# Kernel tuning notes

Hardware: AMD Instinct MI355X
Metric: run time of the kernel (lower is better)

Reference implementation:

```python
import jax, jax.numpy as jnp
import numpy as np

N = 100000   # nodes
E = 1600000  # edges
F = 256      # feature_dim
H = 64       # hidden_dim == out_channels
HEADS = 1


def setup_inputs() -> dict:
    key = jax.random.key(0)
    ks = jax.random.split(key, 12)
    x = jax.random.normal(ks[0], (N, F), dtype=jnp.float32)
    edge_index = jax.random.randint(ks[1], (2, E), 0, N, dtype=jnp.int32)
    s = 0.05
    params = {
        'W_proj': jax.random.normal(ks[2], (F, H), dtype=jnp.float32) * s,
        'b_proj': jnp.zeros((H,), dtype=jnp.float32),
        'Wq1': jax.random.normal(ks[3], (H, HEADS * H), dtype=jnp.float32) * s,
        'Wk1': jax.random.normal(ks[4], (H, HEADS * H), dtype=jnp.float32) * s,
        'Wv1': jax.random.normal(ks[5], (H, HEADS * H), dtype=jnp.float32) * s,
        'Wq2': jax.random.normal(ks[6], (H, HEADS * H), dtype=jnp.float32) * s,
        'Wk2': jax.random.normal(ks[7], (H, HEADS * H), dtype=jnp.float32) * s,
        'Wv2': jax.random.normal(ks[8], (H, HEADS * H), dtype=jnp.float32) * s,
        'W_sig': jax.random.normal(ks[9], (H, 1), dtype=jnp.float32) * s,
        'b_sig': jnp.zeros((1,), dtype=jnp.float32),
    }
    return {'x': x, 'edge_index': edge_index, **params}


def _gat_layer(x, src, dst, Wq, Wk, Wv):
    # x: [N, H]; src/dst: [E] (edge_index[0]=source j, edge_index[1]=dest i)
    n = x.shape[0]
    q = (x @ Wq).reshape(n, HEADS, H)
    k = (x @ Wk).reshape(n, HEADS, H)
    v = (x @ Wv).reshape(n, HEADS, H)
    # edge-wise scores: (q_i * k_j).sum(-1) / sqrt(out_channels)
    scores = jnp.einsum('ehc,ehc->eh', q[dst], k[src]) / np.float32(np.sqrt(H))
    alpha = jax.nn.relu(scores)                                  # [E, HEADS]
    # segment softmax over destination neighborhoods (numerically stable)
    m = jax.ops.segment_max(alpha, dst, num_segments=n)          # [N, HEADS]
    m = jnp.where(jnp.isfinite(m), m, jnp.float32(0.0))
    e = jnp.exp(alpha - m[dst])
    denom = jax.ops.segment_sum(e, dst, num_segments=n)
    a = e / (denom[dst] + jnp.float32(1e-16))                    # [E, HEADS]
    # scatter-weighted sum of values to destinations
    out = jax.ops.segment_sum(v[src] * a[:, :, None], dst, num_segments=n)
    return out.mean(axis=1), a                                   # [N, H], [E, HEADS]


def reference(x, edge_index, W_proj, b_proj, Wq1, Wk1, Wv1, Wq2, Wk2, Wv2, W_sig, b_sig):
    src, dst = edge_index[0], edge_index[1]
    h = jax.nn.gelu(x @ W_proj + b_proj, approximate=False)
    h, attn1 = _gat_layer(h, src, dst, Wq1, Wk1, Wv1)
    h = jax.nn.gelu(h, approximate=False)
    h, attn2 = _gat_layer(h, src, dst, Wq2, Wk2, Wv2)
    signals = h @ W_sig + b_sig                                  # [N, 1]
    return signals, attn1, attn2
```

## Files before the change

### kernel.cpp

```cpp
#include <hip/hip_runtime.h>
#include <hip/hip_fp16.h>
#include <math.h>

#define FF 256
#define HH 64

typedef __attribute__((ext_vector_type(8))) short short8;
typedef __attribute__((ext_vector_type(4))) float f32x4;

__device__ __forceinline__ float gelu_f(float x) {
    float ax = fabsf(x) * 0.70710678118654752f;
    float t = __builtin_amdgcn_rcpf(fmaf(0.3275911f, ax, 1.0f));
    float poly = t * fmaf(t, fmaf(t, fmaf(t, fmaf(t, 1.061405429f, -1.453152027f),
                  1.421413741f), -0.284496736f), 0.254829592f);
    float er = 1.0f - poly * __expf(-ax * ax);
    er = (x < 0.f) ? -er : er;
    return 0.5f * x * (1.0f + er);
}

__device__ __forceinline__ unsigned short bf16rne(float f) {
    unsigned u = __float_as_uint(f);
    unsigned r = u + 0x7FFFu + ((u >> 16) & 1u);
    return (unsigned short)(r >> 16);
}

__device__ __forceinline__ void bf16split(float f, short& hi, short& lo) {
    unsigned u = __float_as_uint(f);
    unsigned r = u + 0x7FFFu + ((u >> 16) & 1u);
    hi = (short)(r >> 16);
    float fh = __uint_as_float(r & 0xFFFF0000u);
    float fl = f - fh;
    unsigned u2 = __float_as_uint(fl);
    unsigned r2 = u2 + 0x7FFFu + ((u2 >> 16) & 1u);
    lo = (short)(r2 >> 16);
}

__device__ __forceinline__ __half2 shfl_xor_h2(__half2 v, int off) {
    union { __half2 h; int i; } u;
    u.h = v;
    u.i = __shfl_xor(u.i, off, 64);
    return u.h;
}

__global__ __launch_bounds__(256) void k_wprep(
        const float* __restrict__ Wp,
        const float* __restrict__ Wq1, const float* __restrict__ Wk1, const float* __restrict__ Wv1,
        const float* __restrict__ Wq2, const float* __restrict__ Wk2, const float* __restrict__ Wv2,
        short* __restrict__ wf) {
    int total = 16384 + 6 * 4096;
    for (int gid = blockIdx.x * 256 + threadIdx.x; gid < total; gid += gridDim.x * 256) {
        const float* W;
        int fid, hibase, lobase;
        if (gid < 16384) {
            W = Wp; fid = gid; hibase = 0; lobase = 16384;
        } else {
            int t = gid - 16384;
            int m = t >> 12;
            fid = t & 4095;
            switch (m) {
                case 0: W = Wq1; break;
                case 1: W = Wk1; break;
                case 2: W = Wv1; break;
                case 3: W = Wq2; break;
                case 4: W = Wk2; break;
                default: W = Wv2; break;
            }
            hibase = 32768 + m * 8192;
            lobase = hibase + 4096;
        }
        int j    = fid & 7;
        int lane = (fid >> 3) & 63;
        int ct   = (fid >> 9) & 3;
        int s    = fid >> 11;
        int k    = s * 32 + (lane >> 4) * 8 + j;
        int col  = ct * 16 + (lane & 15);
        short hi, lo;
        bf16split(W[k * HH + col], hi, lo);
        wf[hibase + fid] = hi;
        wf[lobase + fid] = lo;
    }
}

__device__ __forceinline__ void do_degree(int bid, const int* __restrict__ dst,
        int* __restrict__ deg, int* __restrict__ rank, int E) {
    int e0 = (bid * 256 + threadIdx.x) * 4;
    if (e0 + 3 < E) {
        int4 d4 = *reinterpret_cast<const int4*>(dst + e0);
        int4 r4;
        r4.x = atomicAdd(&deg[d4.x], 1);
        r4.y = atomicAdd(&deg[d4.y], 1);
        r4.z = atomicAdd(&deg[d4.z], 1);
        r4.w = atomicAdd(&deg[d4.w], 1);
        *reinterpret_cast<int4*>(rank + e0) = r4;
    } else {
        for (int e = e0; e < E; ++e) rank[e] = atomicAdd(&deg[dst[e]], 1);
    }
}

__device__ __forceinline__ void do_fill(int bid, const int* __restrict__ src,
        const int* __restrict__ dst, const int* __restrict__ rowptr,
        const int* __restrict__ rank,
        int* __restrict__ esrc, int* __restrict__ inv, int E) {
    int e0 = (bid * 256 + threadIdx.x) * 4;
    if (e0 + 3 < E) {
        int4 d4 = *reinterpret_cast<const int4*>(dst + e0);
        int4 s4 = *reinterpret_cast<const int4*>(src + e0);
        int4 r4 = *reinterpret_cast<const int4*>(rank + e0);
        int p0 = rowptr[d4.x] + r4.x;
        int p1 = rowptr[d4.y] + r4.y;
        int p2 = rowptr[d4.z] + r4.z;
        int p3 = rowptr[d4.w] + r4.w;
        esrc[p0] = s4.x;
        esrc[p1] = s4.y;
        esrc[p2] = s4.z;
        esrc[p3] = s4.w;
        *reinterpret_cast<int4*>(inv + e0) = (int4){p0, p1, p2, p3};
    } else {
        for (int e = e0; e < E; ++e) {
            int pos = rowptr[dst[e]] + rank[e];
            esrc[pos] = src[e];
            inv[e] = pos;
        }
    }
}

__device__ __forceinline__ void do_attn(int bid, const float* __restrict__ ecsr,
        const int* __restrict__ inv, float* __restrict__ attn, int E) {
    int e0 = (bid * 256 + threadIdx.x) * 4;
    if (e0 + 3 < E) {
        int4 i4 = *reinterpret_cast<const int4*>(inv + e0);
        float4 a;
        a.x = ecsr[i4.x]; a.y = ecsr[i4.y]; a.z = ecsr[i4.z]; a.w = ecsr[i4.w];
        *reinterpret_cast<float4*>(attn + e0) = a;
    } else {
        for (int e = e0; e < E; ++e) attn[e] = ecsr[inv[e]];
    }
}

__device__ __forceinline__ void do_proj(int bid, const float* __restrict__ x,
        const short* __restrict__ wf, const float* __restrict__ b,
        float* __restrict__ h, int n) {
    if (bid * 64 >= n) return;
    int lane = threadIdx.x & 63;
    int w    = threadIdx.x >> 6;
    int m    = lane & 15, g = lane >> 4;
    int rowc = min(bid * 64 + w * 16 + m, n - 1);
    const float* xrow = x + (size_t)rowc * FF + g * 8;
    const short* wlo = wf + 16384;
    f32x4 acc[4];
    #pragma unroll
    for (int ct = 0; ct < 4; ++ct) acc[ct] = (f32x4){0.f, 0.f, 0.f, 0.f};
    #pragma unroll
    for (int s = 0; s < 8; ++s) {
        float4 a0 = *reinterpret_cast<const float4*>(xrow + s * 32);
        float4 a1 = *reinterpret_cast<const float4*>(xrow + s * 32 + 4);
        float av[8] = {a0.x, a0.y, a0.z, a0.w, a1.x, a1.y, a1.z, a1.w};
        short8 ah, al;
        #pragma unroll
        for (int j = 0; j < 8; ++j) { short hi, lo; bf16split(av[j], hi, lo); ah[j] = hi; al[j] = lo; }
        #pragma unroll
        for (int ct = 0; ct < 4; ++ct) {
            int fo = ((s * 4 + ct) * 64 + lane) * 8;
            short8 bh = *reinterpret_cast<const short8*>(wf + fo);
            short8 bl = *reinterpret_cast<const short8*>(wlo + fo);
            acc[ct] = __builtin_amdgcn_mfma_f32_16x16x32_bf16(ah, bh, acc[ct], 0, 0, 0);
            acc[ct] = __builtin_amdgcn_mfma_f32_16x16x32_bf16(al, bh, acc[ct], 0, 0, 0);
            acc[ct] = __builtin_amdgcn_mfma_f32_16x16x32_bf16(ah, bl, acc[ct], 0, 0, 0);
        }
    }
    int orow0 = bid * 64 + w * 16 + g * 4;
    #pragma unroll
    for (int ct = 0; ct < 4; ++ct) {
        int col = ct * 16 + m;
        float bias = b[col];
        #pragma unroll
        for (int r = 0; r < 4; ++r) {
            int row = orow0 + r;
            if (row < n) h[(size_t)row * HH + col] = acc[ct][r] + bias;
        }
    }
}

__device__ __forceinline__ void do_qkv(int bid, const float* __restrict__ hsrc,
        const short* __restrict__ wfq, const short* __restrict__ wfk, const short* __restrict__ wfv,
        __half* __restrict__ qh, __half* __restrict__ kv, int n) {
    if (bid * 64 >= n) return;
    int lane = threadIdx.x & 63;
    int w    = threadIdx.x >> 6;
    int m    = lane & 15, g = lane >> 4;
    int rowc = min(bid * 64 + w * 16 + m, n - 1);
    const float* hrow = hsrc + (size_t)rowc * HH + g * 8;
    f32x4 aq[4], ak[4], av_[4];
    #pragma unroll
    for (int ct = 0; ct < 4; ++ct) {
        aq[ct] = (f32x4){0.f, 0.f, 0.f, 0.f};
        ak[ct] = (f32x4){0.f, 0.f, 0.f, 0.f};
        av_[ct] = (f32x4){0.f, 0.f, 0.f, 0.f};
    }
    #pragma unroll
    for (int s = 0; s < 2; ++s) {
        float4 a0 = *reinterpret_cast<const float4*>(hrow + s * 32);
        float4 a1 = *reinterpret_cast<const float4*>(hrow + s * 32 + 4);
        float avv[8] = {a0.x, a0.y, a0.z, a0.w, a1.x, a1.y, a1.z, a1.w};
        short8 ah;
        #pragma unroll
        for (int j = 0; j < 8; ++j) ah[j] = (short)bf16rne(gelu_f(avv[j]));
        #pragma unroll
        for (int ct = 0; ct < 4; ++ct) {
            int fo = ((s * 4 + ct) * 64 + lane) * 8;
            short8 qh8 = *reinterpret_cast<const short8*>(wfq + fo);
            short8 ql8 = *reinterpret_cast<const short8*>(wfq + 4096 + fo);
            short8 kh8 = *reinterpret_cast<const short8*>(wfk + fo);
            short8 kl8 = *reinterpret_cast<const short8*>(wfk + 4096 + fo);
            short8 vh8 = *reinterpret_cast<const short8*>(wfv + fo);
            short8 vl8 = *reinterpret_cast<const short8*>(wfv + 4096 + fo);
            aq[ct] = __builtin_amdgcn_mfma_f32_16x16x32_bf16(ah, qh8, aq[ct], 0, 0, 0);
            aq[ct] = __builtin_amdgcn_mfma_f32_16x16x32_bf16(ah, ql8, aq[ct], 0, 0, 0);
            ak[ct] = __builtin_amdgcn_mfma_f32_16x16x32_bf16(ah, kh8, ak[ct], 0, 0, 0);
            ak[ct] = __builtin_amdgcn_mfma_f32_16x16x32_bf16(ah, kl8, ak[ct], 0, 0, 0);
            av_[ct] = __builtin_amdgcn_mfma_f32_16x16x32_bf16(ah, vh8, av_[ct], 0, 0, 0);
            av_[ct] = __builtin_amdgcn_mfma_f32_16x16x32_bf16(ah, vl8, av_[ct], 0, 0, 0);
        }
    }
    int orow0 = bid * 64 + w * 16 + g * 4;
    #pragma unroll
    for (int ct = 0; ct < 4; ++ct) {
        int col = ct * 16 + m;
        int cb  = (col >> 3) * 16 + (col & 7);
        #pragma unroll
        for (int r = 0; r < 4; ++r) {
            int row = orow0 + r;
            if (row < n) {
                qh[(size_t)row * HH + col]     = __float2half(aq[ct][r]);
                kv[(size_t)row * 128 + cb]     = __float2half(ak[ct][r]);
                kv[(size_t)row * 128 + cb + 8] = __float2half(av_[ct][r]);
            }
        }
    }
}

__global__ __launch_bounds__(256) void k_proj_degree(
        const float* __restrict__ x, const short* __restrict__ wf,
        const float* __restrict__ b, float* __restrict__ h, int n,
        const int* __restrict__ dst, int* __restrict__ deg, int* __restrict__ rank, int E) {
    int bid = blockIdx.x >> 1;
    if ((blockIdx.x & 1) == 0) do_proj(bid, x, wf, b, h, n);
    else                       do_degree(bid, dst, deg, rank, E);
}

__global__ __launch_bounds__(256) void k_qkv_fill(
        const float* __restrict__ hsrc,
        const short* __restrict__ wfq, const short* __restrict__ wfk, const short* __restrict__ wfv,
        __half* __restrict__ qh, __half* __restrict__ kv, int n,
        const int* __restrict__ src, const int* __restrict__ dst,
        const int* __restrict__ rowptr, const int* __restrict__ rank,
        int* __restrict__ esrc, int* __restrict__ inv, int E) {
    int bid = blockIdx.x >> 1;
    if ((blockIdx.x & 1) == 0) do_qkv(bid, hsrc, wfq, wfk, wfv, qh, kv, n);
    else                       do_fill(bid, src, dst, rowptr, rank, esrc, inv, E);
}

__global__ __launch_bounds__(256) void k_qkv_attn(
        const float* __restrict__ hsrc,
        const short* __restrict__ wfq, const short* __restrict__ wfk, const short* __restrict__ wfv,
        __half* __restrict__ qh, __half* __restrict__ kv, int n,
        const float* __restrict__ ecsr, const int* __restrict__ inv,
        float* __restrict__ attn, int E) {
    int bid = blockIdx.x >> 1;
    if ((blockIdx.x & 1) == 0) do_qkv(bid, hsrc, wfq, wfk, wfv, qh, kv, n);
    else                       do_attn(bid, ecsr, inv, attn, E);
}

__global__ __launch_bounds__(256) void k_attn(const float* __restrict__ ecsr,
        const int* __restrict__ inv, float* __restrict__ attn, int E) {
    do_attn(blockIdx.x, ecsr, inv, attn, E);
}

__global__ __launch_bounds__(256) void k_scan1(const int* __restrict__ deg,
        int* __restrict__ out, int* __restrict__ bsums, int n) {
    __shared__ int lds[256];
    int t = threadIdx.x;
    int base = blockIdx.x * 1024 + t * 4;
    int v0 = (base     < n) ? deg[base]     : 0;
    int v1 = (base + 1 < n) ? deg[base + 1] : 0;
    int v2 = (base + 2 < n) ? deg[base + 2] : 0;
    int v3 = (base + 3 < n) ? deg[base + 3] : 0;
    int s = v0 + v1 + v2 + v3;
    int val = s;
    lds[t] = val;
    __syncthreads();
    #pragma unroll
    for (int off = 1; off < 256; off <<= 1) {
        int tmp = (t >= off) ? lds[t - off] : 0;
        __syncthreads();
        val += tmp;
        lds[t] = val;
        __syncthreads();
    }
    if (t == 255) bsums[blockIdx.x] = val;
    int excl = val - s;
    if (base     < n) out[base]     = excl;
    if (base + 1 < n) out[base + 1] = excl + v0;
    if (base + 2 < n) out[base + 2] = excl + v0 + v1;
    if (base + 3 < n) out[base + 3] = excl + v0 + v1 + v2;
}

__global__ __launch_bounds__(256) void k_scan2(const int* __restrict__ bsums,
        int* __restrict__ boffs, int nb) {
    __shared__ int lds[256];
    int t = threadIdx.x;
    int s = (t < nb) ? bsums[t] : 0;
    int val = s;
    lds[t] = val;
    __syncthreads();
    #pragma unroll
    for (int off = 1; off < 256; off <<= 1) {
        int tmp = (t >= off) ? lds[t - off] : 0;
        __syncthreads();
        val += tmp;
        lds[t] = val;
        __syncthreads();
    }
    if (t < nb) boffs[t] = val - s;
}

__global__ __launch_bounds__(256) void k_scan3(int* __restrict__ rowptr,
        const int* __restrict__ boffs, int n, int E) {
    int i = blockIdx.x * 256 + threadIdx.x;
    if (i < n) rowptr[i] += boffs[i >> 10];
    if (i == n) rowptr[n] = E;
}

template<bool LAST>
__global__ __launch_bounds__(256) void k_edge(
        const __half* __restrict__ qarr, const __half* __restrict__ kv,
        const int* __restrict__ rowptr,
        const int* __restrict__ esrc,
        float* __restrict__ ecsr,
        float* __restrict__ hout,
        float* __restrict__ signals,
        const float* __restrict__ Wsig, const float* __restrict__ bsig,
        int n) {
    int node = blockIdx.x * 4 + (threadIdx.x >> 6);
    if (node >= n) return;
    int lane = threadIdx.x & 63;
    int li = lane & 7, g = lane >> 3;
    int start = rowptr[node], end = rowptr[node + 1];
    int deg = end - start;
    __half2 q2[4];
    {
        union { uint4 u; __half2 h[4]; } Q;
        Q.u = *reinterpret_cast<const uint4*>(qarr + (size_t)node * HH + li * 8);
        #pragma unroll
        for (int j = 0; j < 4; ++j) q2[j] = Q.h[j];
    }
    int p0 = start + lane;
    int el = (p0 < end) ? esrc[p0] : 0;

    __half2 acc2[4];
    #pragma unroll
    for (int j = 0; j < 4; ++j) acc2[j] = __float2half2_rn(0.f);
    float s = 0.f;
    for (int c = 0; c < deg; c += 16) {
        int idx0 = c + g, idx1 = c + 8 + g;
        bool v0 = idx0 < deg, v1 = idx1 < deg;
        int sv0, sv1;
        if (c + 16 <= 64) {
            sv0 = __shfl(el, idx0);
            sv1 = __shfl(el, idx1);
        } else {
            sv0 = v0 ? esrc[start + idx0] : 0;
            sv1 = v1 ? esrc[start + idx1] : 0;
        }
        const __half* b0 = kv + (size_t)sv0 * 128 + li * 16;
        const __half* b1 = kv + (size_t)sv1 * 128 + li * 16;
        union { uint4 u; __half2 h[4]; } K0, V0, K1, V1;
        K0.u = *reinterpret_cast<const uint4*>(b0);
        V0.u = *reinterpret_cast<const uint4*>(b0 + 8);
        K1.u = *reinterpret_cast<const uint4*>(b1);
        V1.u = *reinterpret_cast<const uint4*>(b1 + 8);
        __half2 d20 = __float2half2_rn(0.f);
        __half2 d21 = __float2half2_rn(0.f);
        #pragma unroll
        for (int j = 0; j < 4; ++j) {
            d20 = __hfma2(q2[j], K0.h[j], d20);
            d21 = __hfma2(q2[j], K1.h[j], d21);
        }
        float d0 = __low2float(d20) + __high2float(d20);
        float d1 = __low2float(d21) + __high2float(d21);
        d0 += __shfl_xor(d0, 1); d1 += __shfl_xor(d1, 1);
        d0 += __shfl_xor(d0, 2); d1 += __shfl_xor(d1, 2);
        d0 += __shfl_xor(d0, 4); d1 += __shfl_xor(d1, 4);
        float e0 = v0 ? __expf(fmaxf(d0 * 0.125f, 0.f)) : 0.f;
        float e1 = v1 ? __expf(fmaxf(d1 * 0.125f, 0.f)) : 0.f;
        s += e0 + e1;
        if (v0 && li == 0) ecsr[start + idx0] = e0;
        if (v1 && li == 0) ecsr[start + idx1] = e1;
        __half2 e20 = __float2half2_rn(e0);
        __half2 e21 = __float2half2_rn(e1);
        #pragma unroll
        for (int j = 0; j < 4; ++j) {
            acc2[j] = __hfma2(e20, V0.h[j], acc2[j]);
            acc2[j] = __hfma2(e21, V1.h[j], acc2[j]);
        }
    }
    #pragma unroll
    for (int off = 8; off < 64; off <<= 1) {
        s += __shfl_xor(s, off);
        #pragma unroll
        for (int j = 0; j < 4; ++j)
            acc2[j] = __hadd2(acc2[j], shfl_xor_h2(acc2[j], off));
    }
    float inv = 1.0f / (s + 1e-16f);
    float af[8];
    #pragma unroll
    for (int j = 0; j < 4; ++j) {
        af[2 * j]     = __low2float(acc2[j]);
        af[2 * j + 1] = __high2float(acc2[j]);
    }

    if (!LAST) {
        if (g == 0) {
            float4 o0, o1;
            o0.x = af[0] * inv; o0.y = af[1] * inv; o0.z = af[2] * inv; o0.w = af[3] * inv;
            o1.x = af[4] * inv; o1.y = af[5] * inv; o1.z = af[6] * inv; o1.w = af[7] * inv;
            *reinterpret_cast<float4*>(hout + (size_t)node * HH + li * 8)     = o0;
            *reinterpret_cast<float4*>(hout + (size_t)node * HH + li * 8 + 4) = o1;
        }
    } else {
        float4 w0 = *reinterpret_cast<const float4*>(Wsig + li * 8);
        float4 w1 = *reinterpret_cast<const float4*>(Wsig + li * 8 + 4);
        float t = af[0] * w0.x + af[1] * w0.y + af[2] * w0.z + af[3] * w0.w
                + af[4] * w1.x + af[5] * w1.y + af[6] * w1.z + af[7] * w1.w;
        t *= inv;
        t += __shfl_xor(t, 1);
        t += __shfl_xor(t, 2);
        t += __shfl_xor(t, 4);
        if (lane == 0) signals[node] = t + bsig[0];
    }
    for (int p = p0; p < end; p += 64)
        ecsr[p] *= inv;
}

extern "C" void kernel_launch(void* const* d_in, const int* in_sizes, int n_in,
                              void* d_out, int out_size, void* d_ws, size_t ws_size,
                              hipStream_t stream) {
    const float* x   = (const float*)d_in[0];
    const int*   ei  = (const int*)  d_in[1];
    const float* Wp  = (const float*)d_in[2];
    const float* bp  = (const float*)d_in[3];
    const float* Wq1 = (const float*)d_in[4];
    const float* Wk1 = (const float*)d_in[5];
    const float* Wv1 = (const float*)d_in[6];
    const float* Wq2 = (const float*)d_in[7];
    const float* Wk2 = (const float*)d_in[8];
    const float* Wv2 = (const float*)d_in[9];
    const float* Wsg = (const float*)d_in[10];
    const float* bsg = (const float*)d_in[11];

    const int N = in_sizes[0] / FF;
    const int E = in_sizes[1] / 2;
    const int* src = ei;
    const int* dst = ei + E;

    char* ws = (char*)d_ws;
    size_t off = 0;
    auto alloc = [&](size_t bytes) -> void* {
        void* p = ws + off;
        off += (bytes + 255) & ~(size_t)255;
        return p;
    };
    __half* qh   = (__half*)alloc((size_t)N * HH * 2);
    __half* kv   = (__half*)alloc((size_t)N * 128 * 2);
    float* h     = (float*)alloc((size_t)N * HH * 4);
    float* ecsr  = (float*)alloc((size_t)E * 4);
    int* inv     = (int*)alloc((size_t)E * 4);
    int* esrc    = (int*)alloc((size_t)E * 4);
    int* rank    = (int*)alloc((size_t)E * 4);
    int* deg     = (int*)alloc((size_t)N * 4);
    int* rowptr  = (int*)alloc((size_t)(N + 1) * 4);
    int* bsums   = (int*)alloc(256 * 4);
    int* boffs   = (int*)alloc(256 * 4);
    short* wf    = (short*)alloc((size_t)81920 * 2);

    float* out     = (float*)d_out;
    float* signals = out;
    float* attn1   = out + N;
    float* attn2   = out + N + E;

    k_wprep<<<64, 256, 0, stream>>>(Wp, Wq1, Wk1, Wv1, Wq2, Wk2, Wv2, wf);
    hipMemsetAsync(deg, 0, (size_t)N * 4, stream);

    int gemmBlocks = (N + 63) / 64;
    int e4Blocks   = ((E + 3) / 4 + 255) / 256;
    int fused1     = 2 * max(gemmBlocks, e4Blocks);

    k_proj_degree<<<fused1, 256, 0, stream>>>(x, wf, bp, h, N, dst, deg, rank, E);

    int nb = (N + 1023) / 1024;
    k_scan1<<<nb, 256, 0, stream>>>(deg, rowptr, bsums, N);
    k_scan2<<<1, 256, 0, stream>>>(bsums, boffs, nb);
    k_scan3<<<(N + 1 + 255) / 256, 256, 0, stream>>>(rowptr, boffs, N, E);

    const short* wfbase = wf + 32768;
    k_qkv_fill<<<fused1, 256, 0, stream>>>(h, wfbase, wfbase + 8192, wfbase + 16384,
            qh, kv, N, src, dst, rowptr, rank, esrc, inv, E);
    k_edge<false><<<(N + 3) / 4, 256, 0, stream>>>(qh, kv, rowptr, esrc,
            ecsr, h, nullptr, nullptr, nullptr, N);

    k_qkv_attn<<<fused1, 256, 0, stream>>>(h, wfbase + 24576, wfbase + 32768, wfbase + 40960,
            qh, kv, N, ecsr, inv, attn1, E);
    k_edge<true><<<(N + 3) / 4, 256, 0, stream>>>(qh, kv, rowptr, esrc,
            ecsr, nullptr, signals, Wsg, bsg, N);
    k_attn<<<e4Blocks, 256, 0, stream>>>(ecsr, inv, attn2, E);
}
```

Measured before the change: 304.2 us.

## Privatize degree counters per XCD to cut cross-die atomic contention

```diff
diff --git a/kernel.cpp b/kernel.cpp
--- a/kernel.cpp
+++ b/kernel.cpp
@@ -81,35 +81,37 @@
     }
 }
 
-__device__ __forceinline__ void do_degree(int bid, const int* __restrict__ dst,
-        int* __restrict__ deg, int* __restrict__ rank, int E) {
+__device__ __forceinline__ void do_degree(int bid, int p, const int* __restrict__ dst,
+        int* __restrict__ degc, int* __restrict__ rank, int E, int n) {
+    int* deg = degc + p * n;
+    int ptag = p << 24;
     int e0 = (bid * 256 + threadIdx.x) * 4;
     if (e0 + 3 < E) {
         int4 d4 = *reinterpret_cast<const int4*>(dst + e0);
         int4 r4;
-        r4.x = atomicAdd(&deg[d4.x], 1);
-        r4.y = atomicAdd(&deg[d4.y], 1);
-        r4.z = atomicAdd(&deg[d4.z], 1);
-        r4.w = atomicAdd(&deg[d4.w], 1);
+        r4.x = atomicAdd(&deg[d4.x], 1) | ptag;
+        r4.y = atomicAdd(&deg[d4.y], 1) | ptag;
+        r4.z = atomicAdd(&deg[d4.z], 1) | ptag;
+        r4.w = atomicAdd(&deg[d4.w], 1) | ptag;
         *reinterpret_cast<int4*>(rank + e0) = r4;
     } else {
-        for (int e = e0; e < E; ++e) rank[e] = atomicAdd(&deg[dst[e]], 1);
+        for (int e = e0; e < E; ++e) rank[e] = atomicAdd(&deg[dst[e]], 1) | ptag;
     }
 }
 
 __device__ __forceinline__ void do_fill(int bid, const int* __restrict__ src,
-        const int* __restrict__ dst, const int* __restrict__ rowptr,
+        const int* __restrict__ dst, const int* __restrict__ poff,
         const int* __restrict__ rank,
-        int* __restrict__ esrc, int* __restrict__ inv, int E) {
+        int* __restrict__ esrc, int* __restrict__ inv, int E, int n) {
     int e0 = (bid * 256 + threadIdx.x) * 4;
     if (e0 + 3 < E) {
         int4 d4 = *reinterpret_cast<const int4*>(dst + e0);
         int4 s4 = *reinterpret_cast<const int4*>(src + e0);
         int4 r4 = *reinterpret_cast<const int4*>(rank + e0);
-        int p0 = rowptr[d4.x] + r4.x;
-        int p1 = rowptr[d4.y] + r4.y;
-        int p2 = rowptr[d4.z] + r4.z;
-        int p3 = rowptr[d4.w] + r4.w;
+        int p0 = poff[(r4.x >> 24) * n + d4.x] + (r4.x & 0xFFFFFF);
+        int p1 = poff[(r4.y >> 24) * n + d4.y] + (r4.y & 0xFFFFFF);
+        int p2 = poff[(r4.z >> 24) * n + d4.z] + (r4.z & 0xFFFFFF);
+        int p3 = poff[(r4.w >> 24) * n + d4.w] + (r4.w & 0xFFFFFF);
         esrc[p0] = s4.x;
         esrc[p1] = s4.y;
         esrc[p2] = s4.z;
@@ -117,7 +119,8 @@
         *reinterpret_cast<int4*>(inv + e0) = (int4){p0, p1, p2, p3};
     } else {
         for (int e = e0; e < E; ++e) {
-            int pos = rowptr[dst[e]] + rank[e];
+            int r = rank[e];
+            int pos = poff[(r >> 24) * n + dst[e]] + (r & 0xFFFFFF);
             esrc[pos] = src[e];
             inv[e] = pos;
         }
@@ -239,13 +242,19 @@
     }
 }
 
+__device__ __forceinline__ void role_split(int& role, int& sub) {
+    role = (blockIdx.x >> 3) & 1;
+    sub  = ((blockIdx.x >> 4) << 3) | (blockIdx.x & 7);
+}
+
 __global__ __launch_bounds__(256) void k_proj_degree(
         const float* __restrict__ x, const short* __restrict__ wf,
         const float* __restrict__ b, float* __restrict__ h, int n,
-        const int* __restrict__ dst, int* __restrict__ deg, int* __restrict__ rank, int E) {
-    int bid = blockIdx.x >> 1;
-    if ((blockIdx.x & 1) == 0) do_proj(bid, x, wf, b, h, n);
-    else                       do_degree(bid, dst, deg, rank, E);
+        const int* __restrict__ dst, int* __restrict__ degc, int* __restrict__ rank, int E) {
+    int role, sub;
+    role_split(role, sub);
+    if (role == 0) do_proj(sub, x, wf, b, h, n);
+    else           do_degree(sub, blockIdx.x & 7, dst, degc, rank, E, n);
 }
 
 __global__ __launch_bounds__(256) void k_qkv_fill(
@@ -253,11 +262,12 @@
         const short* __restrict__ wfq, const short* __restrict__ wfk, const short* __restrict__ wfv,
         __half* __restrict__ qh, __half* __restrict__ kv, int n,
         const int* __restrict__ src, const int* __restrict__ dst,
-        const int* __restrict__ rowptr, const int* __restrict__ rank,
+        const int* __restrict__ poff, const int* __restrict__ rank,
         int* __restrict__ esrc, int* __restrict__ inv, int E) {
-    int bid = blockIdx.x >> 1;
-    if ((blockIdx.x & 1) == 0) do_qkv(bid, hsrc, wfq, wfk, wfv, qh, kv, n);
-    else                       do_fill(bid, src, dst, rowptr, rank, esrc, inv, E);
+    int role, sub;
+    role_split(role, sub);
+    if (role == 0) do_qkv(sub, hsrc, wfq, wfk, wfv, qh, kv, n);
+    else           do_fill(sub, src, dst, poff, rank, esrc, inv, E, n);
 }
 
 __global__ __launch_bounds__(256) void k_qkv_attn(
@@ -266,9 +276,10 @@
         __half* __restrict__ qh, __half* __restrict__ kv, int n,
         const float* __restrict__ ecsr, const int* __restrict__ inv,
         float* __restrict__ attn, int E) {
-    int bid = blockIdx.x >> 1;
-    if ((blockIdx.x & 1) == 0) do_qkv(bid, hsrc, wfq, wfk, wfv, qh, kv, n);
-    else                       do_attn(bid, ecsr, inv, attn, E);
+    int role, sub;
+    role_split(role, sub);
+    if (role == 0) do_qkv(sub, hsrc, wfq, wfk, wfv, qh, kv, n);
+    else           do_attn(sub, ecsr, inv, attn, E);
 }
 
 __global__ __launch_bounds__(256) void k_attn(const float* __restrict__ ecsr,
@@ -276,16 +287,27 @@
     do_attn(blockIdx.x, ecsr, inv, attn, E);
 }
 
-__global__ __launch_bounds__(256) void k_scan1(const int* __restrict__ deg,
-        int* __restrict__ out, int* __restrict__ bsums, int n) {
+__global__ __launch_bounds__(256) void k_scan1(const int* __restrict__ degc,
+        int* __restrict__ poff, int* __restrict__ out, int* __restrict__ bsums, int n) {
     __shared__ int lds[256];
     int t = threadIdx.x;
     int base = blockIdx.x * 1024 + t * 4;
-    int v0 = (base     < n) ? deg[base]     : 0;
-    int v1 = (base + 1 < n) ? deg[base + 1] : 0;
-    int v2 = (base + 2 < n) ? deg[base + 2] : 0;
-    int v3 = (base + 3 < n) ? deg[base + 3] : 0;
-    int s = v0 + v1 + v2 + v3;
+    int v[4] = {0, 0, 0, 0};
+    #pragma unroll
+    for (int r = 0; r < 4; ++r) {
+        int i = base + r;
+        if (i < n) {
+            int run = 0;
+            #pragma unroll
+            for (int p = 0; p < 8; ++p) {
+                int d = degc[p * n + i];
+                poff[p * n + i] = run;
+                run += d;
+            }
+            v[r] = run;
+        }
+    }
+    int s = v[0] + v[1] + v[2] + v[3];
     int val = s;
     lds[t] = val;
     __syncthreads();
@@ -300,9 +322,9 @@
     if (t == 255) bsums[blockIdx.x] = val;
     int excl = val - s;
     if (base     < n) out[base]     = excl;
-    if (base + 1 < n) out[base + 1] = excl + v0;
-    if (base + 2 < n) out[base + 2] = excl + v0 + v1;
-    if (base + 3 < n) out[base + 3] = excl + v0 + v1 + v2;
+    if (base + 1 < n) out[base + 1] = excl + v[0];
+    if (base + 2 < n) out[base + 2] = excl + v[0] + v[1];
+    if (base + 3 < n) out[base + 3] = excl + v[0] + v[1] + v[2];
 }
 
 __global__ __launch_bounds__(256) void k_scan2(const int* __restrict__ bsums,
@@ -325,9 +347,14 @@
 }
 
 __global__ __launch_bounds__(256) void k_scan3(int* __restrict__ rowptr,
-        const int* __restrict__ boffs, int n, int E) {
+        int* __restrict__ poff, const int* __restrict__ boffs, int n, int E) {
     int i = blockIdx.x * 256 + threadIdx.x;
-    if (i < n) rowptr[i] += boffs[i >> 10];
+    if (i < n) {
+        int r = rowptr[i] + boffs[i >> 10];
+        rowptr[i] = r;
+        #pragma unroll
+        for (int p = 0; p < 8; ++p) poff[p * n + i] += r;
+    }
     if (i == n) rowptr[n] = E;
 }
 
@@ -477,7 +504,8 @@
     int* inv     = (int*)alloc((size_t)E * 4);
     int* esrc    = (int*)alloc((size_t)E * 4);
     int* rank    = (int*)alloc((size_t)E * 4);
-    int* deg     = (int*)alloc((size_t)N * 4);
+    int* degc    = (int*)alloc((size_t)8 * N * 4);
+    int* poff    = (int*)alloc((size_t)8 * N * 4);
     int* rowptr  = (int*)alloc((size_t)(N + 1) * 4);
     int* bsums   = (int*)alloc(256 * 4);
     int* boffs   = (int*)alloc(256 * 4);
@@ -489,26 +517,27 @@
     float* attn2   = out + N + E;
 
     k_wprep<<<64, 256, 0, stream>>>(Wp, Wq1, Wk1, Wv1, Wq2, Wk2, Wv2, wf);
-    hipMemsetAsync(deg, 0, (size_t)N * 4, stream);
+    hipMemsetAsync(degc, 0, (size_t)8 * N * 4, stream);
 
     int gemmBlocks = (N + 63) / 64;
     int e4Blocks   = ((E + 3) / 4 + 255) / 256;
-    int fused1     = 2 * max(gemmBlocks, e4Blocks);
-
-    k_proj_degree<<<fused1, 256, 0, stream>>>(x, wf, bp, h, N, dst, deg, rank, E);
+    int G          = 8 * ((max(gemmBlocks, e4Blocks) + 7) / 8);
+    int fusedGrid  = 2 * G;
+
+    k_proj_degree<<<fusedGrid, 256, 0, stream>>>(x, wf, bp, h, N, dst, degc, rank, E);
 
     int nb = (N + 1023) / 1024;
-    k_scan1<<<nb, 256, 0, stream>>>(deg, rowptr, bsums, N);
+    k_scan1<<<nb, 256, 0, stream>>>(degc, poff, rowptr, bsums, N);
     k_scan2<<<1, 256, 0, stream>>>(bsums, boffs, nb);
-    k_scan3<<<(N + 1 + 255) / 256, 256, 0, stream>>>(rowptr, boffs, N, E);
+    k_scan3<<<(N + 1 + 255) / 256, 256, 0, stream>>>(rowptr, poff, boffs, N, E);
 
     const short* wfbase = wf + 32768;
-    k_qkv_fill<<<fused1, 256, 0, stream>>>(h, wfbase, wfbase + 8192, wfbase + 16384,
-            qh, kv, N, src, dst, rowptr, rank, esrc, inv, E);
+    k_qkv_fill<<<fusedGrid, 256, 0, stream>>>(h, wfbase, wfbase + 8192, wfbase + 16384,
+            qh, kv, N, src, dst, poff, rank, esrc, inv, E);
     k_edge<false><<<(N + 3) / 4, 256, 0, stream>>>(qh, kv, rowptr, esrc,
             ecsr, h, nullptr, nullptr, nullptr, N);
 
-    k_qkv_attn<<<fused1, 256, 0, stream>>>(h, wfbase + 24576, wfbase + 32768, wfbase + 40960,
+    k_qkv_attn<<<fusedGrid, 256, 0, stream>>>(h, wfbase + 24576, wfbase + 32768, wfbase + 40960,
             qh, kv, N, ecsr, inv, attn1, E);
     k_edge<true><<<(N + 3) / 4, 256, 0, stream>>>(qh, kv, rowptr, esrc,
             ecsr, nullptr, signals, Wsg, bsg, N);
```

New measurement: 317.1 us. +4.2%, slower.
